# Performance work log

Hardware: AMD Instinct MI355X
Metric: run time of the kernel (lower is better)

## Reference

```python
import jax, jax.numpy as jnp
import numpy as np

B, T = 4096, 1024
IN, H, N, OUT = 1, 40, 40, 1  # input_size, hidden_size, nr_nodes, output_size
SLOPE = 0.01  # LeakyReLU negative slope (torch default)


def setup_inputs() -> dict:
    key = jax.random.key(0)
    ks = jax.random.split(key, 9)
    s = lambda fan_in: 1.0 / np.sqrt(fan_in)
    u = lambda k, shape, fan_in: jax.random.uniform(k, shape, jnp.float32, -s(fan_in), s(fan_in))
    return {
        "inputs": jax.random.normal(ks[0], (B, T), dtype=jnp.float32),
        # H2H: Linear(41->40), LeakyReLU, Linear(40->40)
        "h2h_w1": u(ks[1], (N, IN + H), IN + H),
        "h2h_b1": u(ks[2], (N,), IN + H),
        "h2h_w2": u(ks[3], (H, N), N),
        "h2h_b2": u(ks[4], (H,), N),
        # H2O: Linear(41->40), LeakyReLU, Linear(40->1)
        "h2o_w1": u(ks[5], (N, IN + H), IN + H),
        "h2o_b1": u(ks[6], (N,), IN + H),
        "h2o_w2": u(ks[7], (OUT, N), N),
        "h2o_b2": u(ks[8], (OUT,), N),
    }


def reference(inputs, h2h_w1, h2h_b1, h2h_w2, h2h_b2, h2o_w1, h2o_b1, h2o_w2, h2o_b2):
    def step(hidden, u_t):
        # combined: [B, 1+H]
        combined = jnp.concatenate([u_t[:, None], hidden], axis=1)
        a = jax.nn.leaky_relu(combined @ h2h_w1.T + h2h_b1, SLOPE)
        hidden_new = a @ h2h_w2.T + h2h_b2                      # [B, H]
        o = jax.nn.leaky_relu(combined @ h2o_w1.T + h2o_b1, SLOPE)
        out_t = (o @ h2o_w2.T + h2o_b2)[:, 0]                   # [B]
        return hidden_new, out_t

    hidden0 = jnp.zeros((inputs.shape[0], H), dtype=inputs.dtype)
    _, ys = jax.lax.scan(step, hidden0, inputs.T)  # ys: [T, B]
    return ys.T  # [B, T]
```

## Files before the change

### kernel.cpp

```cpp
#include <hip/hip_runtime.h>
#include <hip/hip_bf16.h>


#define B_SZ 4096
#define T_SZ 1024
#define HID  40

typedef unsigned short u16;
typedef unsigned int   u32;

__device__ __forceinline__ float bf2f(u16 v) {
  union { u32 u; float f; } c; c.u = ((u32)v) << 16; return c.f;
}

template <bool BF>
__device__ __forceinline__ float ldg(const void* p, long i) {
  if (BF) return bf2f(((const u16*)p)[i]);
  return ((const float*)p)[i];
}

template <bool BF>
__device__ __forceinline__ float4 ldg4(const void* p, long i) {
  float4 r;
  r.x = ldg<BF>(p, i + 0);
  r.y = ldg<BF>(p, i + 1);
  r.z = ldg<BF>(p, i + 2);
  r.w = ldg<BF>(p, i + 3);
  return r;
}

__device__ __forceinline__ bool detect_bf16(const void* w) {
  const u16* p = (const u16*)w;
  bool bf = true;
  for (int i = 0; i < 64; ++i) {
    float f = bf2f(p[i]);
    if (!(fabsf(f) <= 0.2f)) bf = false;
  }
  return bf;
}

__device__ __forceinline__ float pair_other(float x) {
  return __int_as_float(__builtin_amdgcn_update_dpp(
      0, __float_as_int(x), 0xB1, 0xF, 0xF, true));
}

template <bool BF>
__global__ __launch_bounds__(128, 2)
void rnn_kernel(const void* __restrict__ inp,
                const void* __restrict__ h2h_w1, const void* __restrict__ h2h_b1,
                const void* __restrict__ h2h_w2, const void* __restrict__ h2h_b2,
                const void* __restrict__ h2o_w1, const void* __restrict__ h2o_b1,
                const void* __restrict__ h2o_w2, const void* __restrict__ h2o_b2,
                void* __restrict__ out) {
  __shared__ __align__(16) float sH[4][40];
  __shared__ __align__(16) float sA[4][88];

  if (detect_bf16(h2h_w1) != BF) return;

  const int tid  = threadIdx.x;
  const int lane = tid & 63;
  const int wv   = tid >> 6;
  const int el   = (lane >> 4) & 3;
  const int kh   = lane & 1;
  const int wp   = (lane >> 1) & 7;
  const int w    = wv * 8 + wp;
  const int koff = kh * 20;

  float4 wA[5][5];
  float  wu[5], ba[5];
#pragma unroll
  for (int q = 0; q < 5; ++q) {
    const int  j  = 5 * w + q;
    const bool hh = (j < HID);
    const void* w1p = hh ? h2h_w1 : h2o_w1;
    const long  jr  = hh ? j : (j - HID);
    wu[q] = (kh == 0) ? ldg<BF>(w1p, jr * 41) : 0.f;
    ba[q] = (kh == 0) ? ldg<BF>(hh ? h2h_b1 : h2o_b1, jr) : 0.f;
#pragma unroll
    for (int i = 0; i < 5; ++i)
      wA[q][i] = ldg4<BF>(w1p, jr * 41 + 1 + koff + 4 * i);
  }

  const int r2 = (w < 8) ? (32 + w) : ((w == 8) ? 40 : -1);
  float4 wB[3][5];
  float  bb[3] = {0.f, 0.f, 0.f};
#pragma unroll
  for (int q = 0; q < 2; ++q) {
    const long r = w + 16 * q;
    bb[q] = (kh == 0) ? ldg<BF>(h2h_b2, r) : 0.f;
#pragma unroll
    for (int i = 0; i < 5; ++i)
      wB[q][i] = ldg4<BF>(h2h_w2, r * 40 + koff + 4 * i);
  }
  if (r2 == 40) {
    bb[2] = (kh == 0) ? ldg<BF>(h2o_b2, 0) : 0.f;
#pragma unroll
    for (int i = 0; i < 5; ++i)
      wB[2][i] = ldg4<BF>(h2o_w2, koff + 4 * i);
  } else if (r2 >= 0) {
    bb[2] = (kh == 0) ? ldg<BF>(h2h_b2, r2) : 0.f;
#pragma unroll
    for (int i = 0; i < 5; ++i)
      wB[2][i] = ldg4<BF>(h2h_w2, (long)r2 * 40 + koff + 4 * i);
  }

  for (int i = tid; i < 4 * HID; i += 128) ((float*)sH)[i] = 0.f;
  __syncthreads();

  const int  b    = blockIdx.x * 4 + el;
  const long base = (long)b * T_SZ;
  float u_cur = ldg<BF>(inp, base);

  const float4* hp  = (const float4*)(&sH[el][koff]);
  const float4* ap  = (const float4*)(&sA[el][koff]);
  const float4* op  = (const float4*)(&sA[el][40 + koff]);
  float* sAw = &sA[el][5 * w];
  float* sHw = &sH[el][w];

  for (int t = 0; t < T_SZ; ++t) {
    const float u_nxt = (t + 1 < T_SZ) ? ldg<BF>(inp, base + t + 1) : 0.f;

    float4 hv[5];
#pragma unroll
    for (int i = 0; i < 5; ++i) hv[i] = hp[i];
#pragma unroll
    for (int q = 0; q < 5; ++q) {
      float a = fmaf(u_cur, wu[q], ba[q]);
#pragma unroll
      for (int i = 0; i < 5; ++i) {
        a = fmaf(hv[i].x, wA[q][i].x, a);
        a = fmaf(hv[i].y, wA[q][i].y, a);
        a = fmaf(hv[i].z, wA[q][i].z, a);
        a = fmaf(hv[i].w, wA[q][i].w, a);
      }
      const float s   = a + pair_other(a);
      const float act = fmaxf(s, 0.01f * s);
      if (kh == 0) sAw[q] = act;
    }
    __syncthreads();

    float4 av[5];
#pragma unroll
    for (int i = 0; i < 5; ++i) av[i] = ap[i];
#pragma unroll
    for (int q = 0; q < 2; ++q) {
      float s = bb[q];
#pragma unroll
      for (int i = 0; i < 5; ++i) {
        s = fmaf(av[i].x, wB[q][i].x, s);
        s = fmaf(av[i].y, wB[q][i].y, s);
        s = fmaf(av[i].z, wB[q][i].z, s);
        s = fmaf(av[i].w, wB[q][i].w, s);
      }
      const float v = s + pair_other(s);
      if (kh == 0) sHw[16 * q] = v;
    }
    if (r2 >= 0) {
      float s = bb[2];
      if (r2 == 40) {
#pragma unroll
        for (int i = 0; i < 5; ++i) {
          const float4 o4 = op[i];
          s = fmaf(o4.x, wB[2][i].x, s);
          s = fmaf(o4.y, wB[2][i].y, s);
          s = fmaf(o4.z, wB[2][i].z, s);
          s = fmaf(o4.w, wB[2][i].w, s);
        }
        const float v = s + pair_other(s);
        if (kh == 0) {
          if (BF) ((__hip_bfloat16*)out)[base + t] = __float2bfloat16(v);
          else    ((float*)out)[base + t] = v;
        }
      } else {
#pragma unroll
        for (int i = 0; i < 5; ++i) {
          s = fmaf(av[i].x, wB[2][i].x, s);
          s = fmaf(av[i].y, wB[2][i].y, s);
          s = fmaf(av[i].z, wB[2][i].z, s);
          s = fmaf(av[i].w, wB[2][i].w, s);
        }
        const float v = s + pair_other(s);
        if (kh == 0) sH[el][r2] = v;
      }
    }
    __syncthreads();

    u_cur = u_nxt;
  }
}

extern "C" void kernel_launch(void* const* d_in, const int* in_sizes, int n_in,
                              void* d_out, int out_size, void* d_ws, size_t ws_size,
                              hipStream_t stream) {
  (void)in_sizes; (void)n_in; (void)out_size; (void)d_ws; (void)ws_size;
  rnn_kernel<false><<<dim3(B_SZ / 4), dim3(128), 0, stream>>>(
      d_in[0], d_in[1], d_in[2], d_in[3], d_in[4],
      d_in[5], d_in[6], d_in[7], d_in[8], d_out);
  rnn_kernel<true><<<dim3(B_SZ / 4), dim3(128), 0, stream>>>(
      d_in[0], d_in[1], d_in[2], d_in[3], d_in[4],
      d_in[5], d_in[6], d_in[7], d_in[8], d_out);
}
```

Baseline: 904.2 us.

## Use single-wavefront blocks of two batch rows with register-pinned weights

Each block becomes a single 64-lane wavefront that handles 2 batch rows instead of two wavefronts handling 4 rows. The 16 worker pairs per row now live inside one wave, so the per-step __syncthreads barriers only synchronise one wave, making them cheap. Empty asm constraints pin the weight arrays in VGPRs so the compiler does not rematerialise or spill them. The trade-off is that each wave processes fewer rows, so total work per lane rises relative to row throughput, and occupancy depends on the register count.

```diff
diff --git a/kernel.cpp b/kernel.cpp
--- a/kernel.cpp
+++ b/kernel.cpp
@@ -8,6 +8,7 @@
 
 typedef unsigned short u16;
 typedef unsigned int   u32;
+typedef float f4 __attribute__((ext_vector_type(4)));
 
 __device__ __forceinline__ float bf2f(u16 v) {
   union { u32 u; float f; } c; c.u = ((u32)v) << 16; return c.f;
@@ -20,8 +21,8 @@
 }
 
 template <bool BF>
-__device__ __forceinline__ float4 ldg4(const void* p, long i) {
-  float4 r;
+__device__ __forceinline__ f4 ldg4(const void* p, long i) {
+  f4 r;
   r.x = ldg<BF>(p, i + 0);
   r.y = ldg<BF>(p, i + 1);
   r.z = ldg<BF>(p, i + 2);
@@ -45,29 +46,27 @@
 }
 
 template <bool BF>
-__global__ __launch_bounds__(128, 2)
+__global__ __launch_bounds__(64, 2)
 void rnn_kernel(const void* __restrict__ inp,
                 const void* __restrict__ h2h_w1, const void* __restrict__ h2h_b1,
                 const void* __restrict__ h2h_w2, const void* __restrict__ h2h_b2,
                 const void* __restrict__ h2o_w1, const void* __restrict__ h2o_b1,
                 const void* __restrict__ h2o_w2, const void* __restrict__ h2o_b2,
                 void* __restrict__ out) {
-  __shared__ __align__(16) float sH[4][40];
-  __shared__ __align__(16) float sA[4][88];
+  __shared__ __align__(16) float sH[2][48];
+  __shared__ __align__(16) float sA[2][80];
 
   if (detect_bf16(h2h_w1) != BF) return;
 
   const int tid  = threadIdx.x;
   const int lane = tid & 63;
-  const int wv   = tid >> 6;
-  const int el   = (lane >> 4) & 3;
+  const int el   = lane >> 5;
   const int kh   = lane & 1;
-  const int wp   = (lane >> 1) & 7;
-  const int w    = wv * 8 + wp;
+  const int w    = (lane >> 1) & 15;
   const int koff = kh * 20;
 
-  float4 wA[5][5];
-  float  wu[5], ba[5];
+  f4    wA[5][5];
+  float wu[5], ba[5];
 #pragma unroll
   for (int q = 0; q < 5; ++q) {
     const int  j  = 5 * w + q;
@@ -82,8 +81,12 @@
   }
 
   const int r2 = (w < 8) ? (32 + w) : ((w == 8) ? 40 : -1);
-  float4 wB[3][5];
-  float  bb[3] = {0.f, 0.f, 0.f};
+  f4    wB[3][5];
+  float bb[3] = {0.f, 0.f, 0.f};
+#pragma unroll
+  for (int q = 0; q < 3; ++q)
+#pragma unroll
+    for (int i = 0; i < 5; ++i) wB[q][i] = (f4)0.f;
 #pragma unroll
   for (int q = 0; q < 2; ++q) {
     const long r = w + 16 * q;
@@ -104,23 +107,38 @@
       wB[2][i] = ldg4<BF>(h2h_w2, (long)r2 * 40 + koff + 4 * i);
   }
 
-  for (int i = tid; i < 4 * HID; i += 128) ((float*)sH)[i] = 0.f;
+  asm volatile("" :
+      "+v"(wA[0][0]), "+v"(wA[0][1]), "+v"(wA[0][2]), "+v"(wA[0][3]), "+v"(wA[0][4]),
+      "+v"(wA[1][0]), "+v"(wA[1][1]), "+v"(wA[1][2]), "+v"(wA[1][3]), "+v"(wA[1][4]),
+      "+v"(wA[2][0]), "+v"(wA[2][1]), "+v"(wA[2][2]), "+v"(wA[2][3]), "+v"(wA[2][4]),
+      "+v"(wA[3][0]), "+v"(wA[3][1]), "+v"(wA[3][2]), "+v"(wA[3][3]), "+v"(wA[3][4]),
+      "+v"(wA[4][0]), "+v"(wA[4][1]), "+v"(wA[4][2]), "+v"(wA[4][3]), "+v"(wA[4][4]));
+  asm volatile("" :
+      "+v"(wB[0][0]), "+v"(wB[0][1]), "+v"(wB[0][2]), "+v"(wB[0][3]), "+v"(wB[0][4]),
+      "+v"(wB[1][0]), "+v"(wB[1][1]), "+v"(wB[1][2]), "+v"(wB[1][3]), "+v"(wB[1][4]),
+      "+v"(wB[2][0]), "+v"(wB[2][1]), "+v"(wB[2][2]), "+v"(wB[2][3]), "+v"(wB[2][4]));
+  asm volatile("" :
+      "+v"(wu[0]), "+v"(wu[1]), "+v"(wu[2]), "+v"(wu[3]), "+v"(wu[4]),
+      "+v"(ba[0]), "+v"(ba[1]), "+v"(ba[2]), "+v"(ba[3]), "+v"(ba[4]),
+      "+v"(bb[0]), "+v"(bb[1]), "+v"(bb[2]));
+
+  for (int i = tid; i < 2 * 48; i += 64) ((float*)sH)[i] = 0.f;
   __syncthreads();
 
-  const int  b    = blockIdx.x * 4 + el;
+  const int  b    = blockIdx.x * 2 + el;
   const long base = (long)b * T_SZ;
   float u_cur = ldg<BF>(inp, base);
 
-  const float4* hp  = (const float4*)(&sH[el][koff]);
-  const float4* ap  = (const float4*)(&sA[el][koff]);
-  const float4* op  = (const float4*)(&sA[el][40 + koff]);
+  const f4* hp  = (const f4*)(&sH[el][koff]);
+  const f4* ap  = (const f4*)(&sA[el][koff]);
+  const f4* op  = (const f4*)(&sA[el][40 + koff]);
   float* sAw = &sA[el][5 * w];
   float* sHw = &sH[el][w];
 
   for (int t = 0; t < T_SZ; ++t) {
     const float u_nxt = (t + 1 < T_SZ) ? ldg<BF>(inp, base + t + 1) : 0.f;
 
-    float4 hv[5];
+    f4 hv[5];
 #pragma unroll
     for (int i = 0; i < 5; ++i) hv[i] = hp[i];
 #pragma unroll
@@ -139,7 +157,7 @@
     }
     __syncthreads();
 
-    float4 av[5];
+    f4 av[5];
 #pragma unroll
     for (int i = 0; i < 5; ++i) av[i] = ap[i];
 #pragma unroll
@@ -160,7 +178,7 @@
       if (r2 == 40) {
 #pragma unroll
         for (int i = 0; i < 5; ++i) {
-          const float4 o4 = op[i];
+          const f4 o4 = op[i];
           s = fmaf(o4.x, wB[2][i].x, s);
           s = fmaf(o4.y, wB[2][i].y, s);
           s = fmaf(o4.z, wB[2][i].z, s);
@@ -193,10 +211,10 @@
                               void* d_out, int out_size, void* d_ws, size_t ws_size,
                               hipStream_t stream) {
   (void)in_sizes; (void)n_in; (void)out_size; (void)d_ws; (void)ws_size;
-  rnn_kernel<false><<<dim3(B_SZ / 4), dim3(128), 0, stream>>>(
+  rnn_kernel<false><<<dim3(B_SZ / 2), dim3(64), 0, stream>>>(
       d_in[0], d_in[1], d_in[2], d_in[3], d_in[4],
       d_in[5], d_in[6], d_in[7], d_in[8], d_out);
-  rnn_kernel<true><<<dim3(B_SZ / 4), dim3(128), 0, stream>>>(
+  rnn_kernel<true><<<dim3(B_SZ / 2), dim3(64), 0, stream>>>(
       d_in[0], d_in[1], d_in[2], d_in[3], d_in[4],
       d_in[5], d_in[6], d_in[7], d_in[8], d_out);
 }
```

Result: slower. 935.5 us (+3.5%).
